# Optimization experiments

Hardware: AMD Instinct MI355X
Metric: run time of the kernel (lower is better)

## Reference

```python
import jax, jax.numpy as jnp
import numpy as np

N = 100000
E = 1600000
IN_DIM = 128
HID = 32
HEADS = 4
OUT_DIM = 64
NEG_SLOPE = 0.2  # PyG GATConv default LeakyReLU slope


def setup_inputs() -> dict:
    key = jax.random.key(0)
    ks = jax.random.split(key, 10)
    s = 1.0 / np.sqrt(IN_DIM)
    s2 = 1.0 / np.sqrt(HID * HEADS)
    return {
        "x": jax.random.normal(ks[0], (N, IN_DIM), dtype=jnp.float32),
        "edge_index": jax.random.randint(ks[1], (2, E), 0, N, dtype=jnp.int32),
        # layer 1: GATConv(128 -> 32, heads=4)
        "W1": jax.random.normal(ks[2], (IN_DIM, HEADS * HID), dtype=jnp.float32) * s,
        "a_src1": jax.random.normal(ks[3], (HEADS, HID), dtype=jnp.float32) * s,
        "a_dst1": jax.random.normal(ks[4], (HEADS, HID), dtype=jnp.float32) * s,
        "b1": jnp.zeros((HEADS * HID,), dtype=jnp.float32),
        # layer 2: GATConv(128 -> 64, heads=1)
        "W2": jax.random.normal(ks[5], (HEADS * HID, OUT_DIM), dtype=jnp.float32) * s2,
        "a_src2": jax.random.normal(ks[6], (1, OUT_DIM), dtype=jnp.float32) * s2,
        "a_dst2": jax.random.normal(ks[7], (1, OUT_DIM), dtype=jnp.float32) * s2,
        "b2": jnp.zeros((OUT_DIM,), dtype=jnp.float32),
    }


def _gat_conv(x, src, dst, W, a_src, a_dst, b, heads, out_c):
    # x: [N, F] -> h: [N, H, C]
    h = (x @ W).reshape(N, heads, out_c)
    alpha_src = jnp.sum(h * a_src, axis=-1)  # [N, H]
    alpha_dst = jnp.sum(h * a_dst, axis=-1)  # [N, H]
    # per-edge attention logits, softmax grouped by destination node
    e = jax.nn.leaky_relu(alpha_src[src] + alpha_dst[dst], NEG_SLOPE)  # [E', H]
    e_max = jax.ops.segment_max(e, dst, num_segments=N)[dst]
    e_exp = jnp.exp(e - e_max)
    denom = jax.ops.segment_sum(e_exp, dst, num_segments=N)[dst]
    alpha = e_exp / denom  # [E', H]
    msg = h[src] * alpha[..., None]  # [E', H, C]
    out = jax.ops.segment_sum(msg, dst, num_segments=N)  # [N, H, C]
    return out.reshape(N, heads * out_c) + b


def reference(x, edge_index, W1, a_src1, a_dst1, b1, W2, a_src2, a_dst2, b2):
    # PyG GATConv default add_self_loops=True
    loop = jnp.arange(N, dtype=edge_index.dtype)
    src = jnp.concatenate([edge_index[0], loop])
    dst = jnp.concatenate([edge_index[1], loop])
    h = _gat_conv(x, src, dst, W1, a_src1, a_dst1, b1, HEADS, HID)
    h = jax.nn.elu(h)  # dropout omitted (deterministic reference)
    out = _gat_conv(h, src, dst, W2, a_src2, a_dst2, b2, 1, OUT_DIM)
    return out
```

## Files before the change

### kernel.cpp

```cpp
#include <hip/hip_runtime.h>
#include <hip/hip_fp16.h>

#define NNODES 100000
#define NEDGES 1600000
#define INDIM 128
#define HID 32
#define HEADS 4
#define OUTDIM 64
#define NEG_SLOPE 0.2f

__device__ __forceinline__ float lrelu(float x) { return x > 0.f ? x : NEG_SLOPE * x; }

__global__ void k_degree(const int* __restrict__ dst, int* __restrict__ deg, int E) {
    int i = blockIdx.x * blockDim.x + threadIdx.x;
    if (i < E) atomicAdd(&deg[dst[i]], 1);
}

__global__ void k_scanA(const int* __restrict__ deg, int* __restrict__ rowptr,
                        int* __restrict__ bsum, int N) {
    __shared__ int ls[1024];
    int t = threadIdx.x;
    int i = blockIdx.x * 1024 + t;
    int v = (i < N) ? deg[i] : 0;
    ls[t] = v;
    __syncthreads();
    for (int off = 1; off < 1024; off <<= 1) {
        int add = (t >= off) ? ls[t - off] : 0;
        __syncthreads();
        ls[t] += add;
        __syncthreads();
    }
    int incl = ls[t];
    if (i < N) rowptr[i] = incl - v;
    if (t == 1023) bsum[blockIdx.x] = incl;
}

__global__ void k_scanB(const int* __restrict__ bsum, int* __restrict__ boff, int nb) {
    __shared__ int ls[128];
    int t = threadIdx.x;
    int v = (t < nb) ? bsum[t] : 0;
    ls[t] = v;
    __syncthreads();
    for (int off = 1; off < 128; off <<= 1) {
        int add = (t >= off) ? ls[t - off] : 0;
        __syncthreads();
        ls[t] += add;
        __syncthreads();
    }
    if (t < nb) boff[t] = ls[t] - v;
}

__global__ void k_scanC(int* __restrict__ rowptr, int* __restrict__ cursor,
                        const int* __restrict__ boff, int N, int E) {
    int t = threadIdx.x;
    int i = blockIdx.x * 1024 + t;
    if (i < N) {
        int r = rowptr[i] + boff[blockIdx.x];
        rowptr[i] = r;
        cursor[i] = r;
    }
    if (blockIdx.x == 0 && t == 0) rowptr[N] = E;
}

__global__ void k_fill(const int* __restrict__ src, const int* __restrict__ dst,
                       int* __restrict__ cursor, int* __restrict__ csr_src, int E) {
    int i = blockIdx.x * blockDim.x + threadIdx.x;
    if (i < E) {
        int d = dst[i];
        int slot = atomicAdd(&cursor[d], 1);
        csr_src[slot] = src[i];
    }
}

__global__ __launch_bounds__(256) void k_gemm1(const float* __restrict__ x,
                                               const float* __restrict__ W,
                                               __half* __restrict__ h) {
    __shared__ float Ws[INDIM * 128];
    int t = threadIdx.x;
    const float4* W4 = (const float4*)W;
    float4* Ws4 = (float4*)Ws;
    #pragma unroll
    for (int i = t; i < INDIM * 128 / 4; i += 256) Ws4[i] = W4[i];
    __syncthreads();

    int cg = t & 31;
    int rg = t >> 5;
    int r0 = blockIdx.x * 64 + rg * 8;
    const float4* x4 = (const float4*)x;

    int ridx[8];
    #pragma unroll
    for (int rr = 0; rr < 8; ++rr) {
        int r = r0 + rr;
        ridx[rr] = r < NNODES ? r : NNODES - 1;
    }
    float4 acc[8];
    #pragma unroll
    for (int rr = 0; rr < 8; ++rr) acc[rr] = make_float4(0.f, 0.f, 0.f, 0.f);

    for (int k = 0; k < INDIM; k += 4) {
        float4 wv0 = Ws4[(k + 0) * 32 + cg];
        float4 wv1 = Ws4[(k + 1) * 32 + cg];
        float4 wv2 = Ws4[(k + 2) * 32 + cg];
        float4 wv3 = Ws4[(k + 3) * 32 + cg];
        #pragma unroll
        for (int rr = 0; rr < 8; ++rr) {
            float4 xv = x4[(size_t)ridx[rr] * 32 + (k >> 2)];
            acc[rr].x = fmaf(xv.x, wv0.x, fmaf(xv.y, wv1.x, fmaf(xv.z, wv2.x, fmaf(xv.w, wv3.x, acc[rr].x))));
            acc[rr].y = fmaf(xv.x, wv0.y, fmaf(xv.y, wv1.y, fmaf(xv.z, wv2.y, fmaf(xv.w, wv3.y, acc[rr].y))));
            acc[rr].z = fmaf(xv.x, wv0.z, fmaf(xv.y, wv1.z, fmaf(xv.z, wv2.z, fmaf(xv.w, wv3.z, acc[rr].z))));
            acc[rr].w = fmaf(xv.x, wv0.w, fmaf(xv.y, wv1.w, fmaf(xv.z, wv2.w, fmaf(xv.w, wv3.w, acc[rr].w))));
        }
    }
    #pragma unroll
    for (int rr = 0; rr < 8; ++rr) {
        int r = r0 + rr;
        if (r < NNODES) {
            union { __half2 h2[2]; uint2 u; } pk;
            pk.h2[0] = __floats2half2_rn(acc[rr].x, acc[rr].y);
            pk.h2[1] = __floats2half2_rn(acc[rr].z, acc[rr].w);
            ((uint2*)h)[(size_t)r * 32 + cg] = pk.u;
        }
    }
}

__global__ __launch_bounds__(256) void k_gemm2(const float* __restrict__ x,
                                               const float* __restrict__ W,
                                               __half* __restrict__ h) {
    __shared__ float Ws[128 * OUTDIM];
    int t = threadIdx.x;
    const float4* W4 = (const float4*)W;
    float4* Ws4 = (float4*)Ws;
    #pragma unroll
    for (int i = t; i < 128 * OUTDIM / 4; i += 256) Ws4[i] = W4[i];
    __syncthreads();

    int cg = t & 15;
    int rg = t >> 4;
    int r0 = blockIdx.x * 64 + rg * 4;
    const float4* x4 = (const float4*)x;

    int ridx[4];
    #pragma unroll
    for (int rr = 0; rr < 4; ++rr) {
        int r = r0 + rr;
        ridx[rr] = r < NNODES ? r : NNODES - 1;
    }
    float4 acc[4];
    #pragma unroll
    for (int rr = 0; rr < 4; ++rr) acc[rr] = make_float4(0.f, 0.f, 0.f, 0.f);

    for (int k = 0; k < 128; k += 4) {
        float4 wv0 = Ws4[(k + 0) * 16 + cg];
        float4 wv1 = Ws4[(k + 1) * 16 + cg];
        float4 wv2 = Ws4[(k + 2) * 16 + cg];
        float4 wv3 = Ws4[(k + 3) * 16 + cg];
        #pragma unroll
        for (int rr = 0; rr < 4; ++rr) {
            float4 xv = x4[(size_t)ridx[rr] * 32 + (k >> 2)];
            acc[rr].x = fmaf(xv.x, wv0.x, fmaf(xv.y, wv1.x, fmaf(xv.z, wv2.x, fmaf(xv.w, wv3.x, acc[rr].x))));
            acc[rr].y = fmaf(xv.x, wv0.y, fmaf(xv.y, wv1.y, fmaf(xv.z, wv2.y, fmaf(xv.w, wv3.y, acc[rr].y))));
            acc[rr].z = fmaf(xv.x, wv0.z, fmaf(xv.y, wv1.z, fmaf(xv.z, wv2.z, fmaf(xv.w, wv3.z, acc[rr].z))));
            acc[rr].w = fmaf(xv.x, wv0.w, fmaf(xv.y, wv1.w, fmaf(xv.z, wv2.w, fmaf(xv.w, wv3.w, acc[rr].w))));
        }
    }
    #pragma unroll
    for (int rr = 0; rr < 4; ++rr) {
        int r = r0 + rr;
        if (r < NNODES) {
            union { __half2 h2[2]; uint2 u; } pk;
            pk.h2[0] = __floats2half2_rn(acc[rr].x, acc[rr].y);
            pk.h2[1] = __floats2half2_rn(acc[rr].z, acc[rr].w);
            ((uint2*)h)[(size_t)r * 16 + cg] = pk.u;
        }
    }
}

__global__ void k_alpha1(const __half* __restrict__ h, const float* __restrict__ a_src,
                         const float* __restrict__ a_dst, float* __restrict__ asrc,
                         float* __restrict__ adst) {
    int t = threadIdx.x;
    int n = blockIdx.x * 4 + (t >> 6);
    if (n >= NNODES) return;
    int l = t & 63;
    int c0 = 2 * l;
    int head = l >> 4;
    float2 hv = __half22float2(((const __half2*)h)[(size_t)n * 64 + l]);
    int wi = head * HID + (c0 & 31);
    float ps = hv.x * a_src[wi] + hv.y * a_src[wi + 1];
    float pd = hv.x * a_dst[wi] + hv.y * a_dst[wi + 1];
    #pragma unroll
    for (int off = 1; off < 16; off <<= 1) {
        ps += __shfl_xor(ps, off, 16);
        pd += __shfl_xor(pd, off, 16);
    }
    if ((l & 15) == 0) {
        asrc[n * 4 + head] = ps;
        adst[n * 4 + head] = pd;
    }
}

__global__ void k_alpha2(const __half* __restrict__ h, const float* __restrict__ a_src,
                         const float* __restrict__ a_dst, float* __restrict__ asrc,
                         float* __restrict__ adst) {
    int t = threadIdx.x;
    int n = blockIdx.x * 4 + (t >> 6);
    if (n >= NNODES) return;
    int l = t & 63;
    float hv = __half2float(h[(size_t)n * 64 + l]);
    float ps = hv * a_src[l];
    float pd = hv * a_dst[l];
    #pragma unroll
    for (int off = 1; off < 64; off <<= 1) {
        ps += __shfl_xor(ps, off, 64);
        pd += __shfl_xor(pd, off, 64);
    }
    if (l == 0) {
        asrc[n] = ps;
        adst[n] = pd;
    }
}

__global__ __launch_bounds__(256) void k_agg1(const __half* __restrict__ h,
                                              const float* __restrict__ asrc,
                                              const float* __restrict__ adst,
                                              const int* __restrict__ rowptr,
                                              const int* __restrict__ csr_src,
                                              const float* __restrict__ b,
                                              float* __restrict__ out) {
    int t = threadIdx.x;
    int n = blockIdx.x * 4 + (t >> 6);
    if (n >= NNODES) return;
    int l = t & 63;
    int head = l >> 4;
    int c0 = 2 * l;
    const __half2* hh = (const __half2*)h;

    float adsth = adst[n * 4 + head];
    float w = __expf(lrelu(asrc[n * 4 + head] + adsth));
    float2 hv = __half22float2(hh[(size_t)n * 64 + l]);
    float dsum = w;
    float a0 = w * hv.x;
    float a1 = w * hv.y;

    int beg = rowptr[n];
    int end = rowptr[n + 1];
    int p = beg;
    for (; p + 4 <= end; p += 4) {
        int s0 = __builtin_amdgcn_readfirstlane(csr_src[p + 0]);
        int s1 = __builtin_amdgcn_readfirstlane(csr_src[p + 1]);
        int s2 = __builtin_amdgcn_readfirstlane(csr_src[p + 2]);
        int s3 = __builtin_amdgcn_readfirstlane(csr_src[p + 3]);
        float w0 = __expf(lrelu(asrc[(size_t)s0 * 4 + head] + adsth));
        float w1 = __expf(lrelu(asrc[(size_t)s1 * 4 + head] + adsth));
        float w2 = __expf(lrelu(asrc[(size_t)s2 * 4 + head] + adsth));
        float w3 = __expf(lrelu(asrc[(size_t)s3 * 4 + head] + adsth));
        float2 h0 = __half22float2(hh[(size_t)s0 * 64 + l]);
        float2 h1 = __half22float2(hh[(size_t)s1 * 64 + l]);
        float2 h2 = __half22float2(hh[(size_t)s2 * 64 + l]);
        float2 h3 = __half22float2(hh[(size_t)s3 * 64 + l]);
        dsum += (w0 + w1) + (w2 + w3);
        a0 = fmaf(w0, h0.x, a0); a1 = fmaf(w0, h0.y, a1);
        a0 = fmaf(w1, h1.x, a0); a1 = fmaf(w1, h1.y, a1);
        a0 = fmaf(w2, h2.x, a0); a1 = fmaf(w2, h2.y, a1);
        a0 = fmaf(w3, h3.x, a0); a1 = fmaf(w3, h3.y, a1);
    }
    for (; p < end; ++p) {
        int s = __builtin_amdgcn_readfirstlane(csr_src[p]);
        float ws = __expf(lrelu(asrc[(size_t)s * 4 + head] + adsth));
        float2 hs = __half22float2(hh[(size_t)s * 64 + l]);
        dsum += ws;
        a0 = fmaf(ws, hs.x, a0);
        a1 = fmaf(ws, hs.y, a1);
    }
    float inv = 1.0f / dsum;
    float r0 = a0 * inv + b[c0];
    float r1 = a1 * inv + b[c0 + 1];
    r0 = r0 > 0.f ? r0 : __expf(r0) - 1.f;
    r1 = r1 > 0.f ? r1 : __expf(r1) - 1.f;
    *(float2*)&out[(size_t)n * 128 + c0] = make_float2(r0, r1);
}

__global__ __launch_bounds__(256) void k_agg2(const __half* __restrict__ h,
                                              const float* __restrict__ asrc,
                                              const float* __restrict__ adst,
                                              const int* __restrict__ rowptr,
                                              const int* __restrict__ csr_src,
                                              const float* __restrict__ b,
                                              float* __restrict__ out) {
    int t = threadIdx.x;
    int n = blockIdx.x * 4 + (t >> 6);
    if (n >= NNODES) return;
    int l = t & 63;

    float adv = adst[n];
    float w = __expf(lrelu(asrc[n] + adv));
    float dsum = w;
    float acc = w * __half2float(h[(size_t)n * 64 + l]);

    int beg = rowptr[n];
    int end = rowptr[n + 1];
    int p = beg;
    for (; p + 4 <= end; p += 4) {
        int s0 = __builtin_amdgcn_readfirstlane(csr_src[p + 0]);
        int s1 = __builtin_amdgcn_readfirstlane(csr_src[p + 1]);
        int s2 = __builtin_amdgcn_readfirstlane(csr_src[p + 2]);
        int s3 = __builtin_amdgcn_readfirstlane(csr_src[p + 3]);
        float w0 = __expf(lrelu(asrc[s0] + adv));
        float w1 = __expf(lrelu(asrc[s1] + adv));
        float w2 = __expf(lrelu(asrc[s2] + adv));
        float w3 = __expf(lrelu(asrc[s3] + adv));
        float h0 = __half2float(h[(size_t)s0 * 64 + l]);
        float h1 = __half2float(h[(size_t)s1 * 64 + l]);
        float h2 = __half2float(h[(size_t)s2 * 64 + l]);
        float h3 = __half2float(h[(size_t)s3 * 64 + l]);
        dsum += (w0 + w1) + (w2 + w3);
        acc = fmaf(w0, h0, acc);
        acc = fmaf(w1, h1, acc);
        acc = fmaf(w2, h2, acc);
        acc = fmaf(w3, h3, acc);
    }
    for (; p < end; ++p) {
        int s = __builtin_amdgcn_readfirstlane(csr_src[p]);
        float ws = __expf(lrelu(asrc[s] + adv));
        acc = fmaf(ws, __half2float(h[(size_t)s * 64 + l]), acc);
        dsum += ws;
    }
    out[(size_t)n * 64 + l] = acc / dsum + b[l];
}

extern "C" void kernel_launch(void* const* d_in, const int* in_sizes, int n_in,
                              void* d_out, int out_size, void* d_ws, size_t ws_size,
                              hipStream_t stream) {
    const float* x      = (const float*)d_in[0];
    const int*   ei     = (const int*)d_in[1];
    const float* W1     = (const float*)d_in[2];
    const float* a_src1 = (const float*)d_in[3];
    const float* a_dst1 = (const float*)d_in[4];
    const float* b1     = (const float*)d_in[5];
    const float* W2     = (const float*)d_in[6];
    const float* a_src2 = (const float*)d_in[7];
    const float* a_dst2 = (const float*)d_in[8];
    const float* b2     = (const float*)d_in[9];
    float* out = (float*)d_out;

    const int* src = ei;
    const int* dst = ei + NEDGES;

    char* ws = (char*)d_ws;
    size_t off = 0;
    auto alloc = [&](size_t bytes) {
        void* p = ws + off;
        off += (bytes + 255) & ~255ull;
        return p;
    };
    int* rowptr   = (int*)alloc((NNODES + 1) * sizeof(int));
    int* cursor   = (int*)alloc(NNODES * sizeof(int));
    int* csr_src  = (int*)alloc((size_t)NEDGES * sizeof(int));
    __half* h1h   = (__half*)alloc((size_t)NNODES * 128 * sizeof(__half));
    float* eluh   = (float*)alloc((size_t)NNODES * 128 * sizeof(float));
    float* asrc1  = (float*)alloc((size_t)NNODES * 4 * sizeof(float));
    float* adst1  = (float*)alloc((size_t)NNODES * 4 * sizeof(float));
    int* bsum     = (int*)alloc(128 * sizeof(int));
    int* boff     = (int*)alloc(129 * sizeof(int));

    int nb = (NNODES + 1023) / 1024;

    hipMemsetAsync(cursor, 0, NNODES * sizeof(int), stream);
    k_degree<<<(NEDGES + 255) / 256, 256, 0, stream>>>(dst, cursor, NEDGES);
    k_scanA<<<nb, 1024, 0, stream>>>(cursor, rowptr, bsum, NNODES);
    k_scanB<<<1, 128, 0, stream>>>(bsum, boff, nb);
    k_scanC<<<nb, 1024, 0, stream>>>(rowptr, cursor, boff, NNODES, NEDGES);
    k_fill<<<(NEDGES + 255) / 256, 256, 0, stream>>>(src, dst, cursor, csr_src, NEDGES);

    int gn = (NNODES + 3) / 4;

    k_gemm1<<<(NNODES + 63) / 64, 256, 0, stream>>>(x, W1, h1h);
    k_alpha1<<<gn, 256, 0, stream>>>(h1h, a_src1, a_dst1, asrc1, adst1);
    k_agg1<<<gn, 256, 0, stream>>>(h1h, asrc1, adst1, rowptr, csr_src, b1, eluh);

    k_gemm2<<<(NNODES + 63) / 64, 256, 0, stream>>>(eluh, W2, h1h);
    k_alpha2<<<gn, 256, 0, stream>>>(h1h, a_src2, a_dst2, asrc1, adst1);
    k_agg2<<<gn, 256, 0, stream>>>(h1h, asrc1, adst1, rowptr, csr_src, b2, out);
}
```

Measured before the change: 480.5 us.

## Partition CSR fill by destination range and unroll aggregation loops by eight

```diff
diff --git a/kernel.cpp b/kernel.cpp
--- a/kernel.cpp
+++ b/kernel.cpp
@@ -8,6 +8,8 @@
 #define HEADS 4
 #define OUTDIM 64
 #define NEG_SLOPE 0.2f
+#define NRANGES 8
+#define RSIZE (NNODES / NRANGES)
 
 __device__ __forceinline__ float lrelu(float x) { return x > 0.f ? x : NEG_SLOPE * x; }
 
@@ -62,13 +64,24 @@
     if (blockIdx.x == 0 && t == 0) rowptr[N] = E;
 }
 
-__global__ void k_fill(const int* __restrict__ src, const int* __restrict__ dst,
-                       int* __restrict__ cursor, int* __restrict__ csr_src, int E) {
-    int i = blockIdx.x * blockDim.x + threadIdx.x;
-    if (i < E) {
+__global__ __launch_bounds__(256) void k_fill(const int* __restrict__ src,
+                                              const int* __restrict__ dst,
+                                              int* __restrict__ cursor,
+                                              int* __restrict__ csr_src, int E) {
+    int range = blockIdx.x & (NRANGES - 1);
+    int chunk = blockIdx.x >> 3;
+    int nchunks = gridDim.x >> 3;
+    int lo = range * RSIZE;
+    int hi = (range == NRANGES - 1) ? NNODES : lo + RSIZE;
+    int per = (E + nchunks - 1) / nchunks;
+    int beg = chunk * per;
+    int end = min(E, beg + per);
+    for (int i = beg + threadIdx.x; i < end; i += 256) {
         int d = dst[i];
-        int slot = atomicAdd(&cursor[d], 1);
-        csr_src[slot] = src[i];
+        if (d >= lo && d < hi) {
+            int slot = atomicAdd(&cursor[d], 1);
+            csr_src[slot] = src[i];
+        }
     }
 }
 
@@ -246,24 +259,22 @@
     int beg = rowptr[n];
     int end = rowptr[n + 1];
     int p = beg;
-    for (; p + 4 <= end; p += 4) {
-        int s0 = __builtin_amdgcn_readfirstlane(csr_src[p + 0]);
-        int s1 = __builtin_amdgcn_readfirstlane(csr_src[p + 1]);
-        int s2 = __builtin_amdgcn_readfirstlane(csr_src[p + 2]);
-        int s3 = __builtin_amdgcn_readfirstlane(csr_src[p + 3]);
-        float w0 = __expf(lrelu(asrc[(size_t)s0 * 4 + head] + adsth));
-        float w1 = __expf(lrelu(asrc[(size_t)s1 * 4 + head] + adsth));
-        float w2 = __expf(lrelu(asrc[(size_t)s2 * 4 + head] + adsth));
-        float w3 = __expf(lrelu(asrc[(size_t)s3 * 4 + head] + adsth));
-        float2 h0 = __half22float2(hh[(size_t)s0 * 64 + l]);
-        float2 h1 = __half22float2(hh[(size_t)s1 * 64 + l]);
-        float2 h2 = __half22float2(hh[(size_t)s2 * 64 + l]);
-        float2 h3 = __half22float2(hh[(size_t)s3 * 64 + l]);
-        dsum += (w0 + w1) + (w2 + w3);
-        a0 = fmaf(w0, h0.x, a0); a1 = fmaf(w0, h0.y, a1);
-        a0 = fmaf(w1, h1.x, a0); a1 = fmaf(w1, h1.y, a1);
-        a0 = fmaf(w2, h2.x, a0); a1 = fmaf(w2, h2.y, a1);
-        a0 = fmaf(w3, h3.x, a0); a1 = fmaf(w3, h3.y, a1);
+    for (; p + 8 <= end; p += 8) {
+        int s[8];
+        #pragma unroll
+        for (int j = 0; j < 8; ++j) s[j] = __builtin_amdgcn_readfirstlane(csr_src[p + j]);
+        float ww[8];
+        #pragma unroll
+        for (int j = 0; j < 8; ++j) ww[j] = __expf(lrelu(asrc[(size_t)s[j] * 4 + head] + adsth));
+        float2 hx[8];
+        #pragma unroll
+        for (int j = 0; j < 8; ++j) hx[j] = __half22float2(hh[(size_t)s[j] * 64 + l]);
+        #pragma unroll
+        for (int j = 0; j < 8; ++j) {
+            dsum += ww[j];
+            a0 = fmaf(ww[j], hx[j].x, a0);
+            a1 = fmaf(ww[j], hx[j].y, a1);
+        }
     }
     for (; p < end; ++p) {
         int s = __builtin_amdgcn_readfirstlane(csr_src[p]);
@@ -301,24 +312,21 @@
     int beg = rowptr[n];
     int end = rowptr[n + 1];
     int p = beg;
-    for (; p + 4 <= end; p += 4) {
-        int s0 = __builtin_amdgcn_readfirstlane(csr_src[p + 0]);
-        int s1 = __builtin_amdgcn_readfirstlane(csr_src[p + 1]);
-        int s2 = __builtin_amdgcn_readfirstlane(csr_src[p + 2]);
-        int s3 = __builtin_amdgcn_readfirstlane(csr_src[p + 3]);
-        float w0 = __expf(lrelu(asrc[s0] + adv));
-        float w1 = __expf(lrelu(asrc[s1] + adv));
-        float w2 = __expf(lrelu(asrc[s2] + adv));
-        float w3 = __expf(lrelu(asrc[s3] + adv));
-        float h0 = __half2float(h[(size_t)s0 * 64 + l]);
-        float h1 = __half2float(h[(size_t)s1 * 64 + l]);
-        float h2 = __half2float(h[(size_t)s2 * 64 + l]);
-        float h3 = __half2float(h[(size_t)s3 * 64 + l]);
-        dsum += (w0 + w1) + (w2 + w3);
-        acc = fmaf(w0, h0, acc);
-        acc = fmaf(w1, h1, acc);
-        acc = fmaf(w2, h2, acc);
-        acc = fmaf(w3, h3, acc);
+    for (; p + 8 <= end; p += 8) {
+        int s[8];
+        #pragma unroll
+        for (int j = 0; j < 8; ++j) s[j] = __builtin_amdgcn_readfirstlane(csr_src[p + j]);
+        float ww[8];
+        #pragma unroll
+        for (int j = 0; j < 8; ++j) ww[j] = __expf(lrelu(asrc[s[j]] + adv));
+        float hx[8];
+        #pragma unroll
+        for (int j = 0; j < 8; ++j) hx[j] = __half2float(h[(size_t)s[j] * 64 + l]);
+        #pragma unroll
+        for (int j = 0; j < 8; ++j) {
+            dsum += ww[j];
+            acc = fmaf(ww[j], hx[j], acc);
+        }
     }
     for (; p < end; ++p) {
         int s = __builtin_amdgcn_readfirstlane(csr_src[p]);
@@ -371,7 +379,7 @@
     k_scanA<<<nb, 1024, 0, stream>>>(cursor, rowptr, bsum, NNODES);
     k_scanB<<<1, 128, 0, stream>>>(bsum, boff, nb);
     k_scanC<<<nb, 1024, 0, stream>>>(rowptr, cursor, boff, NNODES, NEDGES);
-    k_fill<<<(NEDGES + 255) / 256, 256, 0, stream>>>(src, dst, cursor, csr_src, NEDGES);
+    k_fill<<<NRANGES * 200, 256, 0, stream>>>(src, dst, cursor, csr_src, NEDGES);
 
     int gn = (NNODES + 3) / 4;
 
```

Result: faster. 437.4 us (-9.0%).
